# Kernel optimization log

Measured on AMD Instinct MI355X. Metric: run time of the kernel, lower is better.

## Reference

```python
import jax, jax.numpy as jnp
import numpy as np

B, N, DIM = 4, 2048, 1024
HEADS, DIM_HEAD = 16, 64
SCALE = DIM_HEAD ** -0.5


def setup_inputs() -> dict:
    key = jax.random.key(0)
    ks = jax.random.split(key, 5)
    x = jax.random.normal(ks[0], (B, N, DIM), dtype=jnp.float32)
    s = DIM ** -0.5
    Wq = jax.random.normal(ks[1], (DIM, HEADS * DIM_HEAD), dtype=jnp.float32) * s
    Wk = jax.random.normal(ks[2], (DIM, HEADS * DIM_HEAD), dtype=jnp.float32) * s
    Wv = jax.random.normal(ks[3], (DIM, HEADS * DIM_HEAD), dtype=jnp.float32) * s
    Wo = jax.random.normal(ks[4], (HEADS * DIM_HEAD, DIM), dtype=jnp.float32) * s
    bo = jnp.zeros((DIM,), dtype=jnp.float32)
    return {"x": x, "Wq": Wq, "Wk": Wk, "Wv": Wv, "Wo": Wo, "bo": bo}


def reference(x, Wq, Wk, Wv, Wo, bo):
    b, n, _ = x.shape
    # project and split heads: [b, n, h, d] -> [b, h, n, d]
    def split_heads(t):
        return t.reshape(b, n, HEADS, DIM_HEAD).transpose(0, 2, 1, 3)
    q = split_heads(x @ Wq)
    k = split_heads(x @ Wk)
    v = split_heads(x @ Wv)
    dots = jnp.einsum("bhid,bhjd->bhij", q, k) * SCALE  # [b,h,n,n]
    attn = jax.nn.softmax(dots, axis=-1)
    out = jnp.einsum("bhij,bhjd->bhid", attn, v)  # [b,h,n,d]
    out = out.transpose(0, 2, 1, 3).reshape(b, n, HEADS * DIM_HEAD)
    # project_out is True (heads != 1); dropout is identity at inference
    return out @ Wo + bo
```

## Files before the change

### kernel.cpp

```cpp
#include <hip/hip_runtime.h>
#include <stdint.h>

typedef __attribute__((ext_vector_type(8))) short short8;
typedef __attribute__((ext_vector_type(8))) unsigned short u16x8;
typedef __attribute__((ext_vector_type(4))) float f32x4;

#define DEV static __device__ __forceinline__

DEV unsigned short f2bf(float f) {
  unsigned u = __builtin_bit_cast(unsigned, f);
  u += 0x7FFF + ((u >> 16) & 1);
  return (unsigned short)(u >> 16);
}

DEV unsigned cvtpk_bf16(float lo, float hi) {
  unsigned r;
  asm("v_cvt_pk_bf16_f32 %0, %1, %2" : "=v"(r) : "v"(lo), "v"(hi));
  return r;
}

#define GLOAD16(gptr, lptr)                                                        \
  __builtin_amdgcn_global_load_lds((const __attribute__((address_space(1))) void*)(gptr), \
                                   (__attribute__((address_space(3))) void*)(lptr), 16, 0, 0)

__global__ __launch_bounds__(256) void k_cast_x(const float* __restrict__ in,
                                                unsigned short* __restrict__ out) {
  int idx = (blockIdx.x * 256 + threadIdx.x) * 8;
  float4 a = *(const float4*)(in + idx);
  float4 b = *(const float4*)(in + idx + 4);
  u16x8 v;
  v[0] = f2bf(a.x); v[1] = f2bf(a.y); v[2] = f2bf(a.z); v[3] = f2bf(a.w);
  v[4] = f2bf(b.x); v[5] = f2bf(b.y); v[6] = f2bf(b.z); v[7] = f2bf(b.w);
  *(u16x8*)(out + idx) = v;
}

__global__ __launch_bounds__(256) void k_transW(const float* __restrict__ wq,
                                                const float* __restrict__ wk,
                                                const float* __restrict__ wv,
                                                const float* __restrict__ wo,
                                                unsigned short* __restrict__ wqkvT,
                                                unsigned short* __restrict__ woT) {
  __shared__ __align__(16) unsigned short t[64 * 72];
  int z = blockIdx.z;
  const float* src = (z == 0) ? wq : (z == 1) ? wk : (z == 2) ? wv : wo;
  unsigned short* dst = (z < 3) ? (wqkvT + (size_t)z * 1048576) : woT;
  int r0 = blockIdx.y * 64;
  int c0 = blockIdx.x * 64;
  int tid = threadIdx.x;
#pragma unroll
  for (int it = 0; it < 4; ++it) {
    int idx = it * 256 + tid;
    int il = idx >> 4;
    int c4 = idx & 15;
    float4 v = *(const float4*)(src + (size_t)(r0 + il) * 1024 + c0 + c4 * 4);
    t[(c4 * 4 + 0) * 72 + il] = f2bf(v.x);
    t[(c4 * 4 + 1) * 72 + il] = f2bf(v.y);
    t[(c4 * 4 + 2) * 72 + il] = f2bf(v.z);
    t[(c4 * 4 + 3) * 72 + il] = f2bf(v.w);
  }
  __syncthreads();
#pragma unroll
  for (int it = 0; it < 2; ++it) {
    int idx = it * 256 + tid;
    int ol = idx >> 3;
    int ch = idx & 7;
    *(u16x8*)(dst + (size_t)(c0 + ol) * 1024 + r0 + ch * 8) =
        *(const u16x8*)(t + ol * 72 + ch * 8);
  }
}

template <int MODE>
__global__ __launch_bounds__(256) void k_gemm(const unsigned short* __restrict__ A,
                                              const unsigned short* __restrict__ Bt,
                                              unsigned short* __restrict__ outB,
                                              unsigned short* __restrict__ vTout,
                                              float* __restrict__ outF,
                                              const float* __restrict__ bias) {
  __shared__ __align__(16) unsigned short sA[128 * 64];
  __shared__ __align__(16) unsigned short sB[128 * 64];
  const int tid = threadIdx.x;
  const int l = tid & 63;
  const int w = tid >> 6;

  const int lid = blockIdx.x;
  const int nwg = (MODE == 0) ? 1536 : 512;
  const int swz = (lid & 7) * (nwg >> 3) + (lid >> 3);
  const int z = (MODE == 0) ? (swz >> 9) : 0;
  const int rem = (MODE == 0) ? (swz & 511) : swz;
  const int m0 = (rem >> 3) * 128;
  const int n0 = (rem & 7) * 128;

  const int wm = (w >> 1) * 64;
  const int wn = (w & 1) * 64;
  const int q16 = l & 15, g4 = l >> 4;
  const int lrow = l >> 3;
  const int lsw = ((l & 7) ^ lrow) * 8;

  const unsigned short* bt = Bt + (size_t)z * 1048576;
  unsigned short* dst = outB + (size_t)z * 8388608;
  const float sc = (MODE == 0 && z == 0) ? 0.125f * 1.44269504088896f : 1.0f;

  f32x4 acc[4][4];
#pragma unroll
  for (int i = 0; i < 4; ++i)
#pragma unroll
    for (int j = 0; j < 4; ++j) acc[i][j] = (f32x4){0.f, 0.f, 0.f, 0.f};

  for (int k0 = 0; k0 < 1024; k0 += 64) {
    __syncthreads();
#pragma unroll
    for (int r = 0; r < 4; ++r) {
      int chunk = w * 4 + r;
      int row = chunk * 8 + lrow;
      GLOAD16(A + (size_t)(m0 + row) * 1024 + k0 + lsw, sA + chunk * 512);
      GLOAD16(bt + (size_t)(n0 + row) * 1024 + k0 + lsw, sB + chunk * 512);
    }
    __syncthreads();
#pragma unroll
    for (int kk = 0; kk < 2; ++kk) {
      short8 af[4], bf_[4];
#pragma unroll
      for (int i = 0; i < 4; ++i) {
        int ra = wm + i * 16 + q16;
        af[i] = *(const short8*)(sA + ra * 64 + (((kk * 4 + g4) ^ (ra & 7)) * 8));
        int rb = wn + i * 16 + q16;
        bf_[i] = *(const short8*)(sB + rb * 64 + (((kk * 4 + g4) ^ (rb & 7)) * 8));
      }
#pragma unroll
      for (int mi = 0; mi < 4; ++mi)
#pragma unroll
        for (int ni = 0; ni < 4; ++ni)
          acc[mi][ni] =
              __builtin_amdgcn_mfma_f32_16x16x32_bf16(af[mi], bf_[ni], acc[mi][ni], 0, 0, 0);
    }
  }

  if (MODE == 0 && z == 2) {
#pragma unroll
    for (int mi = 0; mi < 4; ++mi) {
#pragma unroll
      for (int ni = 0; ni < 4; ++ni) {
        int row0 = m0 + wm + mi * 16 + g4 * 4;
        int col = n0 + wn + ni * 16 + q16;
        int b = row0 >> 11, seq0 = row0 & 2047;
        int h = col >> 6, d = col & 63;
        uint2 pv;
        pv.x = cvtpk_bf16(acc[mi][ni][0], acc[mi][ni][1]);
        pv.y = cvtpk_bf16(acc[mi][ni][2], acc[mi][ni][3]);
        *(uint2*)(vTout + (((size_t)(b * 16 + h) * 64 + d) * 2048 + seq0)) = pv;
      }
    }
  } else {
#pragma unroll
    for (int mi = 0; mi < 4; ++mi) {
#pragma unroll
      for (int ni = 0; ni < 4; ++ni) {
#pragma unroll
        for (int j = 0; j < 4; ++j) {
          int row = m0 + wm + mi * 16 + g4 * 4 + j;
          int col = n0 + wn + ni * 16 + q16;
          float val = acc[mi][ni][j];
          if (MODE == 0) {
            val *= sc;
            int b = row >> 11, seq = row & 2047;
            int h = col >> 6, d = col & 63;
            dst[((((size_t)b * 16 + h) * 2048 + seq) << 6) + d] = f2bf(val);
          } else {
            outF[(size_t)row * 1024 + col] = val + bias[col];
          }
        }
      }
    }
  }
}

__global__ __launch_bounds__(512, 4) void k_attn(const unsigned short* __restrict__ Q,
                                                 const unsigned short* __restrict__ Kg,
                                                 const unsigned short* __restrict__ Vt,
                                                 unsigned short* __restrict__ Oo) {
  __shared__ __align__(16) unsigned short sK[2][64 * 64];
  __shared__ __align__(16) unsigned short sV[2][64 * 64];
  __shared__ __align__(16) unsigned short sPa[8][16 * 64];
  __shared__ __align__(16) unsigned short sPb[8][16 * 64];
  const int tid = threadIdx.x;
  const int l = tid & 63, w = tid >> 6;
  const int q16 = l & 15, g = l >> 4;
  const int lrow = l >> 3;
  const int lsw = ((l & 7) ^ lrow) * 8;

  const int bid = blockIdx.x;
  const int swz = (bid & 7) * 64 + (bid >> 3);
  const int bh = swz >> 3;
  const int q0 = (swz & 7) * 256 + w * 32;

  const unsigned short* Qb = Q + ((size_t)bh * 2048 + q0) * 64;
  const unsigned short* Kb = Kg + (size_t)bh * 2048 * 64;
  const unsigned short* Vb = Vt + (size_t)bh * 64 * 2048;

  short8 qfa[2], qfb[2];
#pragma unroll
  for (int s = 0; s < 2; ++s) {
    qfa[s] = *(const short8*)(Qb + q16 * 64 + s * 32 + g * 8);
    qfb[s] = *(const short8*)(Qb + (16 + q16) * 64 + s * 32 + g * 8);
  }

  float suma = 0.f, sumb = 0.f;
  f32x4 oa[4], ob[4];
#pragma unroll
  for (int dt = 0; dt < 4; ++dt) {
    oa[dt] = (f32x4){0.f, 0.f, 0.f, 0.f};
    ob[dt] = (f32x4){0.f, 0.f, 0.f, 0.f};
  }

  auto STAGE = [&](int buf, int kv) {
    int row = w * 8 + lrow;
    GLOAD16(Kb + (size_t)(kv + row) * 64 + lsw, &sK[buf][w * 512]);
    GLOAD16(Vb + (size_t)row * 2048 + kv + lsw, &sV[buf][w * 512]);
  };

  STAGE(0, 0);
  asm volatile("s_waitcnt vmcnt(0)" ::: "memory");
  __syncthreads();

  for (int ti = 0; ti < 32; ++ti) {
    const int cur = ti & 1;
    if (ti < 31) STAGE(cur ^ 1, (ti + 1) * 64);

    f32x4 sta[4], stb[4];
    __builtin_amdgcn_s_setprio(1);
#pragma unroll
    for (int t = 0; t < 4; ++t) {
      sta[t] = (f32x4){0.f, 0.f, 0.f, 0.f};
      stb[t] = (f32x4){0.f, 0.f, 0.f, 0.f};
#pragma unroll
      for (int s = 0; s < 2; ++s) {
        int key = t * 16 + q16;
        short8 kf = *(const short8*)(&sK[cur][key * 64 + (((s * 4 + g) ^ (key & 7)) * 8)]);
        sta[t] = __builtin_amdgcn_mfma_f32_16x16x32_bf16(kf, qfa[s], sta[t], 0, 0, 0);
        stb[t] = __builtin_amdgcn_mfma_f32_16x16x32_bf16(kf, qfb[s], stb[t], 0, 0, 0);
      }
    }
    __builtin_amdgcn_s_setprio(0);

    float pa[4][4], pb[4][4];
    float psa = 0.f, psb = 0.f;
#pragma unroll
    for (int t = 0; t < 4; ++t)
#pragma unroll
      for (int j = 0; j < 4; ++j) {
        pa[t][j] = __builtin_amdgcn_exp2f(sta[t][j]);
        psa += pa[t][j];
        pb[t][j] = __builtin_amdgcn_exp2f(stb[t][j]);
        psb += pb[t][j];
      }
    psa += __shfl_xor(psa, 16);
    psa += __shfl_xor(psa, 32);
    psb += __shfl_xor(psb, 16);
    psb += __shfl_xor(psb, 32);
    suma += psa;
    sumb += psb;

#pragma unroll
    for (int t = 0; t < 4; ++t) {
      int c16 = t * 2 + (g >> 1);
      int off = q16 * 64 + ((c16 ^ (q16 & 7)) * 8) + (g & 1) * 4;
      uint2 pv;
      pv.x = cvtpk_bf16(pa[t][0], pa[t][1]);
      pv.y = cvtpk_bf16(pa[t][2], pa[t][3]);
      *(uint2*)(&sPa[w][off]) = pv;
      pv.x = cvtpk_bf16(pb[t][0], pb[t][1]);
      pv.y = cvtpk_bf16(pb[t][2], pb[t][3]);
      *(uint2*)(&sPb[w][off]) = pv;
    }
    asm volatile("s_waitcnt lgkmcnt(0)" ::: "memory");
    __builtin_amdgcn_sched_barrier(0);

    __builtin_amdgcn_s_setprio(1);
#pragma unroll
    for (int win = 0; win < 2; ++win) {
      int poff = q16 * 64 + (((win * 4 + g) ^ (q16 & 7)) * 8);
      short8 pfa = *(const short8*)(&sPa[w][poff]);
      short8 pfb = *(const short8*)(&sPb[w][poff]);
#pragma unroll
      for (int dt = 0; dt < 4; ++dt) {
        int d = dt * 16 + q16;
        short8 vf = *(const short8*)(&sV[cur][d * 64 + (((win * 4 + g) ^ (d & 7)) * 8)]);
        oa[dt] = __builtin_amdgcn_mfma_f32_16x16x32_bf16(pfa, vf, oa[dt], 0, 0, 0);
        ob[dt] = __builtin_amdgcn_mfma_f32_16x16x32_bf16(pfb, vf, ob[dt], 0, 0, 0);
      }
    }
    __builtin_amdgcn_s_setprio(0);

    asm volatile("s_waitcnt vmcnt(0)" ::: "memory");
    __syncthreads();
  }

  float inva = 1.0f / suma, invb = 1.0f / sumb;
  int b = bh >> 4, h = bh & 15;
#pragma unroll
  for (int j = 0; j < 4; ++j) {
    float ija = __shfl(inva, g * 4 + j);
    float ijb = __shfl(invb, g * 4 + j);
#pragma unroll
    for (int dt = 0; dt < 4; ++dt) {
      sPa[w][(g * 4 + j) * 64 + dt * 16 + q16] = f2bf(oa[dt][j] * ija);
      sPb[w][(g * 4 + j) * 64 + dt * 16 + q16] = f2bf(ob[dt][j] * ijb);
    }
  }
  unsigned short* Ob = Oo + ((size_t)b * 2048 + q0) * 1024 + h * 64;
#pragma unroll
  for (int it = 0; it < 4; ++it) {
    int flat = it * 512 + l * 8;
    int r = flat >> 6, c = flat & 63;
    const unsigned short* src = (it < 2) ? &sPa[w][r * 64 + c] : &sPb[w][(r - 16) * 64 + c];
    *(u16x8*)(Ob + (size_t)r * 1024 + c) = *(const u16x8*)src;
  }
}

extern "C" void kernel_launch(void* const* d_in, const int* in_sizes, int n_in,
                              void* d_out, int out_size, void* d_ws, size_t ws_size,
                              hipStream_t stream) {
  const float* x = (const float*)d_in[0];
  const float* Wq = (const float*)d_in[1];
  const float* Wk = (const float*)d_in[2];
  const float* Wv = (const float*)d_in[3];
  const float* Wo = (const float*)d_in[4];
  const float* bo = (const float*)d_in[5];
  float* out = (float*)d_out;
  char* ws = (char*)d_ws;

  unsigned short* xb    = (unsigned short*)(ws);
  unsigned short* wqkvT = (unsigned short*)(ws + 16777216);
  unsigned short* woT   = (unsigned short*)(ws + 23068672);
  unsigned short* qkv   = (unsigned short*)(ws + 25165824);
  unsigned short* vT    = (unsigned short*)(ws + 75497472);
  unsigned short* aout  = xb;

  k_cast_x<<<4096, 256, 0, stream>>>(x, xb);
  k_transW<<<dim3(16, 16, 4), 256, 0, stream>>>(Wq, Wk, Wv, Wo, wqkvT, woT);
  k_gemm<0><<<1536, 256, 0, stream>>>(xb, wqkvT, qkv, vT, nullptr, nullptr);
  k_attn<<<512, 512, 0, stream>>>(qkv, qkv + 8388608, vT, aout);
  k_gemm<1><<<512, 256, 0, stream>>>(aout, woT, nullptr, nullptr, out, bo);
}
```

Before: 188.3 us.

## Merge prep kernels and halve attention P LDS buffer to raise occupancy

The x cast and weight transpose kernels are merged into one launch to save a kernel launch and its tail. In attention, the two per-warp P staging buffers become one shared buffer: the A tile is written and loaded into registers before the B tile reuses the same space. The epilogue writes the two halves in sequence, and launch bounds go from 4 to 6 blocks per SM. Less LDS and the higher occupancy target aim to hide latency, at the cost of extra LDS wait points and possible register spills under the tighter bound.

```diff
diff --git a/kernel.cpp b/kernel.cpp
--- a/kernel.cpp
+++ b/kernel.cpp
@@ -23,30 +23,33 @@
   __builtin_amdgcn_global_load_lds((const __attribute__((address_space(1))) void*)(gptr), \
                                    (__attribute__((address_space(3))) void*)(lptr), 16, 0, 0)
 
-__global__ __launch_bounds__(256) void k_cast_x(const float* __restrict__ in,
-                                                unsigned short* __restrict__ out) {
-  int idx = (blockIdx.x * 256 + threadIdx.x) * 8;
-  float4 a = *(const float4*)(in + idx);
-  float4 b = *(const float4*)(in + idx + 4);
-  u16x8 v;
-  v[0] = f2bf(a.x); v[1] = f2bf(a.y); v[2] = f2bf(a.z); v[3] = f2bf(a.w);
-  v[4] = f2bf(b.x); v[5] = f2bf(b.y); v[6] = f2bf(b.z); v[7] = f2bf(b.w);
-  *(u16x8*)(out + idx) = v;
-}
-
-__global__ __launch_bounds__(256) void k_transW(const float* __restrict__ wq,
-                                                const float* __restrict__ wk,
-                                                const float* __restrict__ wv,
-                                                const float* __restrict__ wo,
-                                                unsigned short* __restrict__ wqkvT,
-                                                unsigned short* __restrict__ woT) {
+__global__ __launch_bounds__(256) void k_prep(const float* __restrict__ x,
+                                              const float* __restrict__ wq,
+                                              const float* __restrict__ wk,
+                                              const float* __restrict__ wv,
+                                              const float* __restrict__ wo,
+                                              unsigned short* __restrict__ xb,
+                                              unsigned short* __restrict__ wqkvT,
+                                              unsigned short* __restrict__ woT) {
   __shared__ __align__(16) unsigned short t[64 * 72];
-  int z = blockIdx.z;
+  const int bid = blockIdx.x;
+  const int tid = threadIdx.x;
+  if (bid < 4096) {
+    int idx = (bid * 256 + tid) * 8;
+    float4 a = *(const float4*)(x + idx);
+    float4 b = *(const float4*)(x + idx + 4);
+    u16x8 v;
+    v[0] = f2bf(a.x); v[1] = f2bf(a.y); v[2] = f2bf(a.z); v[3] = f2bf(a.w);
+    v[4] = f2bf(b.x); v[5] = f2bf(b.y); v[6] = f2bf(b.z); v[7] = f2bf(b.w);
+    *(u16x8*)(xb + idx) = v;
+    return;
+  }
+  const int tt = bid - 4096;
+  const int z = tt >> 8;
+  const int r0 = ((tt >> 4) & 15) * 64;
+  const int c0 = (tt & 15) * 64;
   const float* src = (z == 0) ? wq : (z == 1) ? wk : (z == 2) ? wv : wo;
   unsigned short* dst = (z < 3) ? (wqkvT + (size_t)z * 1048576) : woT;
-  int r0 = blockIdx.y * 64;
-  int c0 = blockIdx.x * 64;
-  int tid = threadIdx.x;
 #pragma unroll
   for (int it = 0; it < 4; ++it) {
     int idx = it * 256 + tid;
@@ -174,14 +177,13 @@
   }
 }
 
-__global__ __launch_bounds__(512, 4) void k_attn(const unsigned short* __restrict__ Q,
+__global__ __launch_bounds__(512, 6) void k_attn(const unsigned short* __restrict__ Q,
                                                  const unsigned short* __restrict__ Kg,
                                                  const unsigned short* __restrict__ Vt,
                                                  unsigned short* __restrict__ Oo) {
   __shared__ __align__(16) unsigned short sK[2][64 * 64];
   __shared__ __align__(16) unsigned short sV[2][64 * 64];
-  __shared__ __align__(16) unsigned short sPa[8][16 * 64];
-  __shared__ __align__(16) unsigned short sPb[8][16 * 64];
+  __shared__ __align__(16) unsigned short sP[8][16 * 64];
   const int tid = threadIdx.x;
   const int l = tid & 63, w = tid >> 6;
   const int q16 = l & 15, g = l >> 4;
@@ -267,27 +269,37 @@
       uint2 pv;
       pv.x = cvtpk_bf16(pa[t][0], pa[t][1]);
       pv.y = cvtpk_bf16(pa[t][2], pa[t][3]);
-      *(uint2*)(&sPa[w][off]) = pv;
+      *(uint2*)(&sP[w][off]) = pv;
+    }
+    asm volatile("s_waitcnt lgkmcnt(0)" ::: "memory");
+    __builtin_amdgcn_sched_barrier(0);
+    short8 pfa0 = *(const short8*)(&sP[w][q16 * 64 + ((g ^ (q16 & 7)) * 8)]);
+    short8 pfa1 = *(const short8*)(&sP[w][q16 * 64 + (((4 + g) ^ (q16 & 7)) * 8)]);
+    __builtin_amdgcn_sched_barrier(0);
+#pragma unroll
+    for (int t = 0; t < 4; ++t) {
+      int c16 = t * 2 + (g >> 1);
+      int off = q16 * 64 + ((c16 ^ (q16 & 7)) * 8) + (g & 1) * 4;
+      uint2 pv;
       pv.x = cvtpk_bf16(pb[t][0], pb[t][1]);
       pv.y = cvtpk_bf16(pb[t][2], pb[t][3]);
-      *(uint2*)(&sPb[w][off]) = pv;
+      *(uint2*)(&sP[w][off]) = pv;
     }
     asm volatile("s_waitcnt lgkmcnt(0)" ::: "memory");
     __builtin_amdgcn_sched_barrier(0);
+    short8 pfb0 = *(const short8*)(&sP[w][q16 * 64 + ((g ^ (q16 & 7)) * 8)]);
+    short8 pfb1 = *(const short8*)(&sP[w][q16 * 64 + (((4 + g) ^ (q16 & 7)) * 8)]);
 
     __builtin_amdgcn_s_setprio(1);
 #pragma unroll
-    for (int win = 0; win < 2; ++win) {
-      int poff = q16 * 64 + (((win * 4 + g) ^ (q16 & 7)) * 8);
-      short8 pfa = *(const short8*)(&sPa[w][poff]);
-      short8 pfb = *(const short8*)(&sPb[w][poff]);
-#pragma unroll
-      for (int dt = 0; dt < 4; ++dt) {
-        int d = dt * 16 + q16;
-        short8 vf = *(const short8*)(&sV[cur][d * 64 + (((win * 4 + g) ^ (d & 7)) * 8)]);
-        oa[dt] = __builtin_amdgcn_mfma_f32_16x16x32_bf16(pfa, vf, oa[dt], 0, 0, 0);
-        ob[dt] = __builtin_amdgcn_mfma_f32_16x16x32_bf16(pfb, vf, ob[dt], 0, 0, 0);
-      }
+    for (int dt = 0; dt < 4; ++dt) {
+      int d = dt * 16 + q16;
+      short8 vf0 = *(const short8*)(&sV[cur][d * 64 + ((g ^ (d & 7)) * 8)]);
+      oa[dt] = __builtin_amdgcn_mfma_f32_16x16x32_bf16(pfa0, vf0, oa[dt], 0, 0, 0);
+      ob[dt] = __builtin_amdgcn_mfma_f32_16x16x32_bf16(pfb0, vf0, ob[dt], 0, 0, 0);
+      short8 vf1 = *(const short8*)(&sV[cur][d * 64 + (((4 + g) ^ (d & 7)) * 8)]);
+      oa[dt] = __builtin_amdgcn_mfma_f32_16x16x32_bf16(pfa1, vf1, oa[dt], 0, 0, 0);
+      ob[dt] = __builtin_amdgcn_mfma_f32_16x16x32_bf16(pfb1, vf1, ob[dt], 0, 0, 0);
     }
     __builtin_amdgcn_s_setprio(0);
 
@@ -297,23 +309,37 @@
 
   float inva = 1.0f / suma, invb = 1.0f / sumb;
   int b = bh >> 4, h = bh & 15;
+  unsigned short* Ob = Oo + ((size_t)b * 2048 + q0) * 1024 + h * 64;
 #pragma unroll
   for (int j = 0; j < 4; ++j) {
     float ija = __shfl(inva, g * 4 + j);
-    float ijb = __shfl(invb, g * 4 + j);
-#pragma unroll
-    for (int dt = 0; dt < 4; ++dt) {
-      sPa[w][(g * 4 + j) * 64 + dt * 16 + q16] = f2bf(oa[dt][j] * ija);
-      sPb[w][(g * 4 + j) * 64 + dt * 16 + q16] = f2bf(ob[dt][j] * ijb);
-    }
-  }
-  unsigned short* Ob = Oo + ((size_t)b * 2048 + q0) * 1024 + h * 64;
-#pragma unroll
-  for (int it = 0; it < 4; ++it) {
+#pragma unroll
+    for (int dt = 0; dt < 4; ++dt)
+      sP[w][(g * 4 + j) * 64 + dt * 16 + q16] = f2bf(oa[dt][j] * ija);
+  }
+  asm volatile("s_waitcnt lgkmcnt(0)" ::: "memory");
+  __builtin_amdgcn_sched_barrier(0);
+#pragma unroll
+  for (int it = 0; it < 2; ++it) {
     int flat = it * 512 + l * 8;
     int r = flat >> 6, c = flat & 63;
-    const unsigned short* src = (it < 2) ? &sPa[w][r * 64 + c] : &sPb[w][(r - 16) * 64 + c];
-    *(u16x8*)(Ob + (size_t)r * 1024 + c) = *(const u16x8*)src;
+    *(u16x8*)(Ob + (size_t)r * 1024 + c) = *(const u16x8*)(&sP[w][r * 64 + c]);
+  }
+  __builtin_amdgcn_sched_barrier(0);
+#pragma unroll
+  for (int j = 0; j < 4; ++j) {
+    float ijb = __shfl(invb, g * 4 + j);
+#pragma unroll
+    for (int dt = 0; dt < 4; ++dt)
+      sP[w][(g * 4 + j) * 64 + dt * 16 + q16] = f2bf(ob[dt][j] * ijb);
+  }
+  asm volatile("s_waitcnt lgkmcnt(0)" ::: "memory");
+  __builtin_amdgcn_sched_barrier(0);
+#pragma unroll
+  for (int it = 0; it < 2; ++it) {
+    int flat = it * 512 + l * 8;
+    int r = flat >> 6, c = flat & 63;
+    *(u16x8*)(Ob + (size_t)(16 + r) * 1024 + c) = *(const u16x8*)(&sP[w][r * 64 + c]);
   }
 }
 
@@ -336,8 +362,7 @@
   unsigned short* vT    = (unsigned short*)(ws + 75497472);
   unsigned short* aout  = xb;
 
-  k_cast_x<<<4096, 256, 0, stream>>>(x, xb);
-  k_transW<<<dim3(16, 16, 4), 256, 0, stream>>>(Wq, Wk, Wv, Wo, wqkvT, woT);
+  k_prep<<<5120, 256, 0, stream>>>(x, Wq, Wk, Wv, Wo, xb, wqkvT, woT);
   k_gemm<0><<<1536, 256, 0, stream>>>(xb, wqkvT, qkv, vT, nullptr, nullptr);
   k_attn<<<512, 512, 0, stream>>>(qkv, qkv + 8388608, vT, aout);
   k_gemm<1><<<512, 256, 0, stream>>>(aout, woT, nullptr, nullptr, out, bo);
```

Result: slower. 457.8 us (+143.1%).
